# Kernel tuning notes

Hardware: AMD Instinct MI355X
Metric: run time of the kernel (lower is better)

Reference implementation:

```python
import jax, jax.numpy as jnp
import numpy as np

D_MODEL = 1024
N_HEADS = 16
D_K = D_MODEL // N_HEADS
RANK = 16
LORA_SCALING = 32.0 / RANK  # alpha / rank = 2.0
LN_EPS = 1e-5


def _lora_linear(x, w, b, A, B):
    # torch nn.Linear: x @ w.T + b ; LoRA: (x @ A @ B) * scaling
    return x @ w.T + b + (x @ A @ B) * LORA_SCALING


def setup_inputs() -> dict:
    key = jax.random.key(0)
    ks = jax.random.split(key, 20)
    d = {}
    d['x'] = jax.random.normal(ks[0], (4, 1024, D_MODEL), dtype=jnp.float32)
    i = 1
    for p in ('q', 'k', 'v', 'o'):
        d[f'{p}_w'] = jax.random.normal(ks[i], (D_MODEL, D_MODEL), dtype=jnp.float32) * (1.0 / np.sqrt(D_MODEL)); i += 1
        d[f'{p}_b'] = jax.random.normal(ks[i], (D_MODEL,), dtype=jnp.float32) * 0.01; i += 1
        d[f'{p}_A'] = jax.random.normal(ks[i], (D_MODEL, RANK), dtype=jnp.float32) * 0.01; i += 1
        d[f'{p}_B'] = jax.random.normal(ks[i], (RANK, D_MODEL), dtype=jnp.float32) * 0.01; i += 1
    d['ln_g'] = jnp.ones((D_MODEL,), dtype=jnp.float32)
    d['ln_b'] = jnp.zeros((D_MODEL,), dtype=jnp.float32)
    return d


def reference(x, q_w, q_b, q_A, q_B, k_w, k_b, k_A, k_B,
              v_w, v_b, v_A, v_B, o_w, o_b, o_A, o_B, ln_g, ln_b):
    B, S, _ = x.shape
    # QKV projections with LoRA, reshape to [B, H, S, d_k]
    def split_heads(t):
        return t.reshape(B, S, N_HEADS, D_K).transpose(0, 2, 1, 3)
    Q = split_heads(_lora_linear(x, q_w, q_b, q_A, q_B))
    K = split_heads(_lora_linear(x, k_w, k_b, k_A, k_B))
    V = split_heads(_lora_linear(x, v_w, v_b, v_A, v_B))

    scores = jnp.einsum('bhqd,bhkd->bhqk', Q, K) / jnp.sqrt(jnp.float32(D_K))
    attn = jax.nn.softmax(scores, axis=-1)  # dropout is identity in eval
    ctx = jnp.einsum('bhqk,bhkd->bhqd', attn, V)
    ctx = ctx.transpose(0, 2, 1, 3).reshape(B, S, D_MODEL)

    out = _lora_linear(ctx, o_w, o_b, o_A, o_B)
    # residual + LayerNorm
    h = out + x
    mu = jnp.mean(h, axis=-1, keepdims=True)
    var = jnp.mean(jnp.square(h - mu), axis=-1, keepdims=True)
    normed = (h - mu) * jax.lax.rsqrt(var + LN_EPS) * ln_g + ln_b
    return normed, attn.mean(axis=1)
```

## Files before the change

### kernel.cpp

```cpp
#include <hip/hip_runtime.h>

#define DMODEL 1024
#define NHEADS 16
#define DHEAD  64
#define RANK   16
#define BATCH  4
#define SEQ    1024
#define MTOT   (BATCH*SEQ)
#define QSCALE 0.18033688011112042f

typedef __bf16 bf16;
typedef __bf16 bf16x8 __attribute__((ext_vector_type(8)));
typedef __bf16 bf16x4 __attribute__((ext_vector_type(4)));
typedef float  f32x4  __attribute__((ext_vector_type(4)));

__device__ __forceinline__ int swz128(int row, int byte_in_row) {
  int slot = byte_in_row >> 4;
  return row * 128 + (((slot ^ (row & 7)) << 4) | (byte_in_row & 15));
}

__device__ __forceinline__ void gll16(const void* g, void* l) {
  __builtin_amdgcn_global_load_lds((const __attribute__((address_space(1))) unsigned int*)g,
                                   (__attribute__((address_space(3))) unsigned int*)l, 16, 0, 0);
}

#define TRRD(lo, hi, base, o0, o1)                                   \
  asm volatile("ds_read_b64_tr_b16 %0, %2 offset:" #o0 "\n\t"        \
               "ds_read_b64_tr_b16 %1, %2 offset:" #o1               \
               : "=v"(lo), "=v"(hi) : "v"(base));

__global__ void prep_weff_kernel(
    const float* __restrict__ W0, const float* __restrict__ A0, const float* __restrict__ B0,
    const float* __restrict__ W1, const float* __restrict__ A1, const float* __restrict__ B1,
    const float* __restrict__ W2, const float* __restrict__ A2, const float* __restrict__ B2,
    const float* __restrict__ W3, const float* __restrict__ A3, const float* __restrict__ B3,
    bf16* __restrict__ out) {
  const int l = blockIdx.y;
  const float* W = l == 0 ? W0 : l == 1 ? W1 : l == 2 ? W2 : W3;
  const float* A = l == 0 ? A0 : l == 1 ? A1 : l == 2 ? A2 : A3;
  const float* Bm = l == 0 ? B0 : l == 1 ? B1 : l == 2 ? B2 : B3;
  out += (size_t)l * DMODEL * DMODEL;
  const int n = blockIdx.x;
  __shared__ float bsc[RANK];
  if (threadIdx.x < RANK) bsc[threadIdx.x] = Bm[threadIdx.x * DMODEL + n] * 2.0f;
  __syncthreads();
  float br[RANK];
#pragma unroll
  for (int r = 0; r < RANK; ++r) br[r] = bsc[r];
  for (int k0 = 0; k0 < DMODEL; k0 += 256) {
    int k = k0 + threadIdx.x;
    float acc = W[n * DMODEL + k];
    const float4* arow = (const float4*)(A + k * RANK);
#pragma unroll
    for (int r4 = 0; r4 < 4; ++r4) {
      float4 a = arow[r4];
      acc += a.x*br[r4*4+0] + a.y*br[r4*4+1] + a.z*br[r4*4+2] + a.w*br[r4*4+3];
    }
    out[n * DMODEL + k] = (bf16)acc;
  }
}

__global__ void cast_x_kernel(const float* __restrict__ x, bf16* __restrict__ xb) {
  int i = (blockIdx.x * blockDim.x + threadIdx.x) * 4;
  float4 v = *(const float4*)(x + i);
  bf16x4 o = { (bf16)v.x, (bf16)v.y, (bf16)v.z, (bf16)v.w };
  *(bf16x4*)(xb + i) = o;
}

__device__ __forceinline__ void gemm_core64(
    const bf16* __restrict__ Ain, const bf16* __restrict__ Bin,
    char* sA, char* sB, int m0, int n0, f32x4 (&acc)[2][4]) {
  const int tid = threadIdx.x;
  const int w = tid >> 6, lane = tid & 63;
  const int wm = (w & 1) * 32, wn = (w >> 1) * 64;
  const bf16* pA[2]; char* lA[2];
  const bf16* pB[4]; char* lB[4];
#pragma unroll
  for (int i = 0; i < 2; ++i) {
    int chunk = i * 4 + w;
    int row = chunk * 8 + (lane >> 3);
    int ss = (lane & 7) ^ (row & 7);
    pA[i] = Ain + (size_t)(m0 + row) * DMODEL + ss * 8;
    lA[i] = sA + chunk * 1024;
  }
#pragma unroll
  for (int i = 0; i < 4; ++i) {
    int chunk = i * 4 + w;
    int row = chunk * 8 + (lane >> 3);
    int ss = (lane & 7) ^ (row & 7);
    pB[i] = Bin + (size_t)(n0 + row) * DMODEL + ss * 8;
    lB[i] = sB + chunk * 1024;
  }
  for (int kt = 0; kt < DMODEL / 64; ++kt) {
    const int kbase = kt * 64;
#pragma unroll
    for (int i = 0; i < 2; ++i) gll16(pA[i] + kbase, lA[i]);
#pragma unroll
    for (int i = 0; i < 4; ++i) gll16(pB[i] + kbase, lB[i]);
    __syncthreads();
#pragma unroll
    for (int ks = 0; ks < 2; ++ks) {
      bf16x8 af[2], bfg[4];
#pragma unroll
      for (int mi = 0; mi < 2; ++mi)
        af[mi] = *(const bf16x8*)(sA + swz128(wm + mi*16 + (lane & 15), ks*64 + (lane >> 4)*16));
#pragma unroll
      for (int ni = 0; ni < 4; ++ni)
        bfg[ni] = *(const bf16x8*)(sB + swz128(wn + ni*16 + (lane & 15), ks*64 + (lane >> 4)*16));
#pragma unroll
      for (int mi = 0; mi < 2; ++mi)
#pragma unroll
        for (int ni = 0; ni < 4; ++ni)
          acc[mi][ni] = __builtin_amdgcn_mfma_f32_16x16x32_bf16(af[mi], bfg[ni], acc[mi][ni], 0, 0, 0);
    }
    __syncthreads();
  }
}

__global__ __launch_bounds__(256) void gemm_qkv_kernel(
    const bf16* __restrict__ xb, const bf16* __restrict__ weff,
    const float* __restrict__ bq, const float* __restrict__ bk, const float* __restrict__ bv,
    bf16* __restrict__ Qb, bf16* __restrict__ Kb, bf16* __restrict__ Vb)
{
  __shared__ __align__(16) char sA[8192];
  __shared__ __align__(16) char sB[16384];
  const int tid = threadIdx.x, w = tid >> 6, lane = tid & 63;
  const int bid = blockIdx.x;
  const int nb = (bid & 7) * 192 + (bid >> 3);
  const int n0 = (nb % 24) * 128, m0 = (nb / 24) * 64;
  const int z = n0 >> 10;
  const float* bias = z == 0 ? bq : z == 1 ? bk : bv;
  bf16* outp = z == 0 ? Qb : (z == 1 ? Kb : Vb);
  const float scl = z == 0 ? QSCALE : 1.0f;
  const int wm = (w & 1) * 32, wn = (w >> 1) * 64;
  f32x4 acc[2][4] = {};
  gemm_core64(xb, weff, sA, sB, m0, n0, acc);
#pragma unroll
  for (int mi = 0; mi < 2; ++mi) {
#pragma unroll
    for (int ni = 0; ni < 4; ++ni) {
      int col = n0 + wn + ni * 16 + (lane & 15);
      float bcol = bias[col & 1023];
      int h = (col >> 6) & 15, d = col & 63;
#pragma unroll
      for (int r = 0; r < 4; ++r) {
        int row = m0 + wm + mi * 16 + (lane >> 4) * 4 + r;
        float v = (acc[mi][ni][r] + bcol) * scl;
        int b = row >> 10, s = row & 1023;
        outp[(size_t)((b * NHEADS + h) * SEQ + s) * DHEAD + d] = (bf16)v;
      }
    }
  }
}

__global__ __launch_bounds__(256) void gemm_o_kernel(
    const bf16* __restrict__ ctx, const bf16* __restrict__ weff,
    const float* __restrict__ bias, const float* __restrict__ resid,
    float* __restrict__ outf)
{
  __shared__ __align__(16) char sA[8192];
  __shared__ __align__(16) char sB[16384];
  const int tid = threadIdx.x, w = tid >> 6, lane = tid & 63;
  const int bid = blockIdx.x;
  const int nb = (bid & 7) * 64 + (bid >> 3);
  const int n0 = (nb & 7) * 128, m0 = (nb >> 3) * 64;
  const int wm = (w & 1) * 32, wn = (w >> 1) * 64;
  f32x4 acc[2][4] = {};
  gemm_core64(ctx, weff, sA, sB, m0, n0, acc);
#pragma unroll
  for (int mi = 0; mi < 2; ++mi) {
#pragma unroll
    for (int ni = 0; ni < 4; ++ni) {
      int col = n0 + wn + ni * 16 + (lane & 15);
      float bcol = bias[col];
#pragma unroll
      for (int r = 0; r < 4; ++r) {
        int row = m0 + wm + mi * 16 + (lane >> 4) * 4 + r;
        outf[(size_t)row * DMODEL + col] =
            acc[mi][ni][r] + bcol + resid[(size_t)row * DMODEL + col];
      }
    }
  }
}

__global__ __launch_bounds__(512) void flash_kernel(
    const bf16* __restrict__ Qb, const bf16* __restrict__ Kb, const bf16* __restrict__ Vb,
    bf16* __restrict__ ctx, float* __restrict__ lstat)
{
  __shared__ __align__(16) char sK[8192];
  __shared__ __align__(16) char sV[8192];
  __shared__ __align__(16) char sP[8 * 2048];
  const int tid = threadIdx.x, w = tid >> 6, lane = tid & 63;
  const int bid = blockIdx.x;
  const int nb = (bid & 7) * 64 + (bid >> 3);
  const int bh = nb >> 3;
  const int q0 = (nb & 7) * 128;
  const bf16* Qbase = Qb + (size_t)bh * SEQ * DHEAD;
  const bf16* Kbase = Kb + (size_t)bh * SEQ * DHEAD;
  const bf16* Vbase = Vb + (size_t)bh * SEQ * DHEAD;
  const int qw = q0 + w * 16;

  bf16x8 aq[2];
#pragma unroll
  for (int ks = 0; ks < 2; ++ks)
    aq[ks] = *(const bf16x8*)(Qbase + (size_t)(qw + (lane & 15)) * DHEAD + ks * 32 + (lane >> 4) * 8);

  const bf16* pK; const bf16* pV; char* lK; char* lV;
  {
    int ci = w;
    int rowK = ci * 8 + (lane >> 3);
    int ssK = (lane & 7) ^ (rowK & 7);
    pK = Kbase + (size_t)rowK * DHEAD + ssK * 8;
    lK = sK + ci * 1024;
    int kV = ci * 8 + ((lane >> 5) & 1) * 4 + ((lane >> 1) & 3);
    int dV = (((lane >> 3) & 3) << 4) + ((lane & 1) << 3);
    pV = Vbase + (size_t)kV * DHEAD + dV;
    lV = sV + ci * 1024;
  }

  char* sPw = sP + w * 2048;
  const unsigned pbase = (unsigned)(uintptr_t)sPw + ((lane >> 4) << 8) + ((lane & 15) << 3);
  const unsigned vbase0 = (unsigned)(uintptr_t)sV + ((lane >> 4) << 10) + ((lane & 15) << 3);
  char* pwr = sPw + ((lane >> 4) << 3) + (lane & 15) * 32;

  f32x4 cacc[4] = {};
  float lsum[4] = {0.f, 0.f, 0.f, 0.f};

  for (int kt = 0; kt < SEQ / 64; ++kt) {
    const size_t kofs = (size_t)(kt * 64) * DHEAD;
    gll16(pK + kofs, lK);
    gll16(pV + kofs, lV);
    __syncthreads();

    f32x4 sc[4] = {};
#pragma unroll
    for (int ks = 0; ks < 2; ++ks)
#pragma unroll
      for (int ni = 0; ni < 4; ++ni) {
        bf16x8 bk = *(const bf16x8*)(sK + swz128(ni*16 + (lane & 15), ks*64 + (lane >> 4)*16));
        sc[ni] = __builtin_amdgcn_mfma_f32_16x16x32_bf16(aq[ks], bk, sc[ni], 0, 0, 0);
      }

#pragma unroll
    for (int ni = 0; ni < 4; ++ni) {
      float p0 = __builtin_amdgcn_exp2f(sc[ni][0]);
      float p1 = __builtin_amdgcn_exp2f(sc[ni][1]);
      float p2 = __builtin_amdgcn_exp2f(sc[ni][2]);
      float p3 = __builtin_amdgcn_exp2f(sc[ni][3]);
      lsum[0] += p0; lsum[1] += p1; lsum[2] += p2; lsum[3] += p3;
      bf16x4 pb = { (bf16)p0, (bf16)p1, (bf16)p2, (bf16)p3 };
      *(bf16x4*)(pwr + ni * 512) = pb;
    }
    asm volatile("s_waitcnt lgkmcnt(0)" ::: "memory");

    unsigned long long t0, t1, v0[4], v1[4];
    TRRD(t0, t1, pbase, 0, 128)
    TRRD(v0[0], v1[0], vbase0, 0, 512)
    TRRD(v0[1], v1[1], vbase0, 128, 640)
    TRRD(v0[2], v1[2], vbase0, 256, 768)
    TRRD(v0[3], v1[3], vbase0, 384, 896)
    asm volatile("s_waitcnt lgkmcnt(0)" ::: "memory");
    __builtin_amdgcn_sched_barrier(0);
    {
      union { unsigned long long u[2]; bf16x8 v; } pu, vu;
      pu.u[0] = t0; pu.u[1] = t1;
#pragma unroll
      for (int ni = 0; ni < 4; ++ni) {
        vu.u[0] = v0[ni]; vu.u[1] = v1[ni];
        cacc[ni] = __builtin_amdgcn_mfma_f32_16x16x32_bf16(pu.v, vu.v, cacc[ni], 0, 0, 0);
      }
    }
    TRRD(t0, t1, pbase, 1024, 1152)
    TRRD(v0[0], v1[0], vbase0, 4096, 4608)
    TRRD(v0[1], v1[1], vbase0, 4224, 4736)
    TRRD(v0[2], v1[2], vbase0, 4352, 4864)
    TRRD(v0[3], v1[3], vbase0, 4480, 4992)
    asm volatile("s_waitcnt lgkmcnt(0)" ::: "memory");
    __builtin_amdgcn_sched_barrier(0);
    {
      union { unsigned long long u[2]; bf16x8 v; } pu, vu;
      pu.u[0] = t0; pu.u[1] = t1;
#pragma unroll
      for (int ni = 0; ni < 4; ++ni) {
        vu.u[0] = v0[ni]; vu.u[1] = v1[ni];
        cacc[ni] = __builtin_amdgcn_mfma_f32_16x16x32_bf16(pu.v, vu.v, cacc[ni], 0, 0, 0);
      }
    }
    __syncthreads();
  }

#pragma unroll
  for (int r = 0; r < 4; ++r) {
#pragma unroll
    for (int off = 1; off < 16; off <<= 1) lsum[r] += __shfl_xor(lsum[r], off);
  }

  const int b = bh >> 4, hh = bh & 15;
#pragma unroll
  for (int r = 0; r < 4; ++r) {
    float inv = __builtin_amdgcn_rcpf(lsum[r]);
    int qrow = qw + (lane >> 4) * 4 + r;
#pragma unroll
    for (int ni = 0; ni < 4; ++ni) {
      int d = ni * 16 + (lane & 15);
      ctx[(size_t)(b * SEQ + qrow) * DMODEL + hh * DHEAD + d] = (bf16)(cacc[ni][r] * inv);
    }
    if ((lane & 15) == 0) lstat[(size_t)bh * SEQ + qrow] = lsum[r];
  }
}

__global__ __launch_bounds__(256) void mean_kernel(
    const bf16* __restrict__ Qb, const bf16* __restrict__ Kb,
    const float* __restrict__ lstat, float* __restrict__ out2)
{
  __shared__ __align__(16) char sK[2 * 16384];
  const int tid = threadIdx.x, w = tid >> 6, lane = tid & 63;
  const int bid = blockIdx.x;
  const int nb2 = (bid & 7) * 64 + (bid >> 3);
  const int b = nb2 >> 7;
  const int q0 = ((nb2 >> 3) & 15) * 64, k0 = (nb2 & 7) * 128;
  const int qw = q0 + w * 16;
  size_t goff[4]; int lofs[4];
#pragma unroll
  for (int i = 0; i < 4; ++i) {
    int chunk = i * 4 + w;
    int row = chunk * 8 + (lane >> 3);
    int ss = (lane & 7) ^ (row & 7);
    goff[i] = (size_t)(k0 + row) * DHEAD + ss * 8;
    lofs[i] = chunk * 1024;
  }
  const bf16* Kb_b = Kb + (size_t)b * NHEADS * SEQ * DHEAD;
  const bf16* Qb_b = Qb + (size_t)b * NHEADS * SEQ * DHEAD;

  f32x4 macc[8] = {};
#pragma unroll
  for (int i = 0; i < 4; ++i) gll16(Kb_b + goff[i], sK + lofs[i]);
  asm volatile("s_waitcnt vmcnt(0)" ::: "memory");
  __syncthreads();

  for (int h = 0; h < NHEADS; ++h) {
    const int cur = (h & 1) << 14, nxt = cur ^ 16384;
    if (h + 1 < NHEADS) {
      const bf16* Kn = Kb_b + (size_t)(h + 1) * SEQ * DHEAD;
#pragma unroll
      for (int i = 0; i < 4; ++i) gll16(Kn + goff[i], sK + nxt + lofs[i]);
    }
    const bf16* Qbase = Qb_b + (size_t)h * SEQ * DHEAD;
    bf16x8 aq[2];
#pragma unroll
    for (int ks = 0; ks < 2; ++ks)
      aq[ks] = *(const bf16x8*)(Qbase + (size_t)(qw + (lane & 15)) * DHEAD
                                + ks * 32 + (lane >> 4) * 8);
    char* cK = sK + cur;
    f32x4 sc[8] = {};
#pragma unroll
    for (int ks = 0; ks < 2; ++ks)
#pragma unroll
      for (int ni = 0; ni < 8; ++ni) {
        bf16x8 bk = *(const bf16x8*)(cK + swz128(ni*16 + (lane & 15), ks*64 + (lane >> 4)*16));
        sc[ni] = __builtin_amdgcn_mfma_f32_16x16x32_bf16(aq[ks], bk, sc[ni], 0, 0, 0);
      }
    float lsc[4];
    const float* ls = lstat + ((size_t)(b * NHEADS + h)) * SEQ;
#pragma unroll
    for (int r = 0; r < 4; ++r)
      lsc[r] = 0.0625f * __builtin_amdgcn_rcpf(ls[qw + (lane >> 4)*4 + r]);
#pragma unroll
    for (int ni = 0; ni < 8; ++ni)
#pragma unroll
      for (int r = 0; r < 4; ++r)
        macc[ni][r] += __builtin_amdgcn_exp2f(sc[ni][r]) * lsc[r];
    asm volatile("s_waitcnt vmcnt(0)" ::: "memory");
    __syncthreads();
  }
#pragma unroll
  for (int r = 0; r < 4; ++r) {
    int qrow = qw + (lane >> 4) * 4 + r;
#pragma unroll
    for (int ni = 0; ni < 8; ++ni)
      out2[(size_t)(b * SEQ + qrow) * SEQ + k0 + ni * 16 + (lane & 15)] = macc[ni][r];
  }
}

__global__ __launch_bounds__(256) void ln_kernel(
    float* __restrict__ hb, const float* __restrict__ g,
    const float* __restrict__ bvec, float* __restrict__ out)
{
  const int row = blockIdx.x, t = threadIdx.x;
  float4 v = *(const float4*)(hb + (size_t)row * DMODEL + t * 4);
  float s = v.x + v.y + v.z + v.w;
  float s2 = v.x*v.x + v.y*v.y + v.z*v.z + v.w*v.w;
#pragma unroll
  for (int off = 32; off >= 1; off >>= 1) {
    s  += __shfl_down(s, off);
    s2 += __shfl_down(s2, off);
  }
  __shared__ float red[8];
  const int w = t >> 6;
  if ((t & 63) == 0) { red[w] = s; red[4 + w] = s2; }
  __syncthreads();
  if (t == 0) {
    red[0] = red[0] + red[1] + red[2] + red[3];
    red[4] = red[4] + red[5] + red[6] + red[7];
  }
  __syncthreads();
  float mu = red[0] * (1.0f / DMODEL);
  float var = red[4] * (1.0f / DMODEL) - mu * mu;
  float rs = rsqrtf(var + 1e-5f);
  float4 gv = *(const float4*)(g + t * 4);
  float4 bv = *(const float4*)(bvec + t * 4);
  float4 o;
  o.x = (v.x - mu) * rs * gv.x + bv.x;
  o.y = (v.y - mu) * rs * gv.y + bv.y;
  o.z = (v.z - mu) * rs * gv.z + bv.z;
  o.w = (v.w - mu) * rs * gv.w + bv.w;
  *(float4*)(out + (size_t)row * DMODEL + t * 4) = o;
}

extern "C" void kernel_launch(void* const* d_in, const int* in_sizes, int n_in,
                              void* d_out, int out_size, void* d_ws, size_t ws_size,
                              hipStream_t stream) {
  (void)in_sizes; (void)n_in; (void)out_size; (void)ws_size;
  const float* x = (const float*)d_in[0];
  const float* w_[4]  = {(const float*)d_in[1],  (const float*)d_in[5],
                         (const float*)d_in[9],  (const float*)d_in[13]};
  const float* b_[4]  = {(const float*)d_in[2],  (const float*)d_in[6],
                         (const float*)d_in[10], (const float*)d_in[14]};
  const float* A_[4]  = {(const float*)d_in[3],  (const float*)d_in[7],
                         (const float*)d_in[11], (const float*)d_in[15]};
  const float* Bm_[4] = {(const float*)d_in[4],  (const float*)d_in[8],
                         (const float*)d_in[12], (const float*)d_in[16]};
  const float* lng = (const float*)d_in[17];
  const float* lnb = (const float*)d_in[18];

  char* ws = (char*)d_ws;
  bf16* xb    = (bf16*)(ws);
  bf16* weff  = (bf16*)(ws + (8u  << 20));
  bf16* Qb    = (bf16*)(ws + (16u << 20));
  bf16* Kb    = (bf16*)(ws + (24u << 20));
  bf16* Vb    = (bf16*)(ws + (32u << 20));
  float* lstat = (float*)(ws + (40u << 20));
  bf16* ctx = xb;
  float* hbuf = (float*)d_out;
  float* out2 = (float*)d_out + (size_t)MTOT * DMODEL;

  prep_weff_kernel<<<dim3(DMODEL, 4), dim3(256), 0, stream>>>(
      w_[0], A_[0], Bm_[0], w_[1], A_[1], Bm_[1],
      w_[2], A_[2], Bm_[2], w_[3], A_[3], Bm_[3], weff);
  cast_x_kernel<<<dim3(MTOT * DMODEL / 1024), dim3(256), 0, stream>>>(x, xb);

  gemm_qkv_kernel<<<dim3(1536), 256, 0, stream>>>(
      xb, weff, b_[0], b_[1], b_[2], Qb, Kb, Vb);

  flash_kernel<<<dim3(512), 512, 0, stream>>>(Qb, Kb, Vb, ctx, lstat);
  mean_kernel<<<dim3(512), 256, 0, stream>>>(Qb, Kb, lstat, out2);
  gemm_o_kernel<<<dim3(512), 256, 0, stream>>>(
      ctx, weff + 3u * DMODEL * DMODEL, b_[3], x, hbuf);
  ln_kernel<<<dim3(MTOT), 256, 0, stream>>>(hbuf, lng, lnb, hbuf);
}
```

Before: 144.5 us.

## Double-buffer K/V tiles in flash kernel and enlarge QKV GEMM tile

The flash attention kernel now keeps two LDS buffers for K and V. It prefetches the next 64-key tile with global_load_lds while the current tile is consumed, which hides global load latency and removes one barrier per iteration. The QKV projection GEMM moves from a 64x128 tile with 256 threads to a 128x128 tile with 512 threads (8 waves). That raises operand reuse per block and halves the grid. The cost is doubled LDS use in flash (32 KB extra) and fewer, larger GEMM blocks, which may lower occupancy.

Result: no change. 142.9 us (-1.1%).

```diff
diff --git a/kernel.cpp b/kernel.cpp
--- a/kernel.cpp
+++ b/kernel.cpp
@@ -67,6 +67,79 @@
   *(bf16x4*)(xb + i) = o;
 }
 
+__global__ __launch_bounds__(512) void gemm_qkv_kernel(
+    const bf16* __restrict__ xb, const bf16* __restrict__ weff,
+    const float* __restrict__ bq, const float* __restrict__ bk, const float* __restrict__ bv,
+    bf16* __restrict__ Qb, bf16* __restrict__ Kb, bf16* __restrict__ Vb)
+{
+  __shared__ __align__(16) char sA[16384];
+  __shared__ __align__(16) char sB[16384];
+  const int tid = threadIdx.x, w = tid >> 6, lane = tid & 63;
+  const int bid = blockIdx.x;
+  const int nb = (bid & 7) * 96 + (bid >> 3);
+  const int n0 = (nb % 24) * 128, m0 = (nb / 24) * 128;
+  const int z = n0 >> 10;
+  const float* bias = z == 0 ? bq : z == 1 ? bk : bv;
+  bf16* outp = z == 0 ? Qb : (z == 1 ? Kb : Vb);
+  const float scl = z == 0 ? QSCALE : 1.0f;
+  const int wm = (w & 3) * 32, wn = (w >> 2) * 64;
+  f32x4 acc[2][4] = {};
+
+  const bf16* pA[2]; const bf16* pB[2]; char* lA[2]; char* lB[2];
+#pragma unroll
+  for (int i = 0; i < 2; ++i) {
+    int ci = i * 8 + w;
+    int row = ci * 8 + (lane >> 3);
+    int ss = (lane & 7) ^ (row & 7);
+    pA[i] = xb + (size_t)(m0 + row) * DMODEL + ss * 8;
+    pB[i] = weff + (size_t)(n0 + row) * DMODEL + ss * 8;
+    lA[i] = sA + ci * 1024;
+    lB[i] = sB + ci * 1024;
+  }
+  for (int kt = 0; kt < DMODEL / 64; ++kt) {
+    const int kbase = kt * 64;
+#pragma unroll
+    for (int i = 0; i < 2; ++i) {
+      gll16(pA[i] + kbase, lA[i]);
+      gll16(pB[i] + kbase, lB[i]);
+    }
+    __syncthreads();
+#pragma unroll
+    for (int ks = 0; ks < 2; ++ks) {
+      bf16x8 af[2], bfg[4];
+#pragma unroll
+      for (int mi = 0; mi < 2; ++mi)
+        af[mi] = *(const bf16x8*)(sA + swz128(wm + mi*16 + (lane & 15), ks*64 + (lane >> 4)*16));
+#pragma unroll
+      for (int ni = 0; ni < 4; ++ni)
+        bfg[ni] = *(const bf16x8*)(sB + swz128(wn + ni*16 + (lane & 15), ks*64 + (lane >> 4)*16));
+#pragma unroll
+      for (int mi = 0; mi < 2; ++mi)
+#pragma unroll
+        for (int ni = 0; ni < 4; ++ni)
+          acc[mi][ni] = __builtin_amdgcn_mfma_f32_16x16x32_bf16(af[mi], bfg[ni], acc[mi][ni], 0, 0, 0);
+    }
+    __syncthreads();
+  }
+
+#pragma unroll
+  for (int mi = 0; mi < 2; ++mi) {
+#pragma unroll
+    for (int ni = 0; ni < 4; ++ni) {
+      int col = n0 + wn + ni * 16 + (lane & 15);
+      float bcol = bias[col & 1023];
+      int h = (col >> 6) & 15, d = col & 63;
+#pragma unroll
+      for (int r = 0; r < 4; ++r) {
+        int row = m0 + wm + mi * 16 + (lane >> 4) * 4 + r;
+        float v = (acc[mi][ni][r] + bcol) * scl;
+        int b = row >> 10, s = row & 1023;
+        outp[(size_t)((b * NHEADS + h) * SEQ + s) * DHEAD + d] = (bf16)v;
+      }
+    }
+  }
+}
+
 __device__ __forceinline__ void gemm_core64(
     const bf16* __restrict__ Ain, const bf16* __restrict__ Bin,
     char* sA, char* sB, int m0, int n0, f32x4 (&acc)[2][4]) {
@@ -114,42 +187,6 @@
           acc[mi][ni] = __builtin_amdgcn_mfma_f32_16x16x32_bf16(af[mi], bfg[ni], acc[mi][ni], 0, 0, 0);
     }
     __syncthreads();
-  }
-}
-
-__global__ __launch_bounds__(256) void gemm_qkv_kernel(
-    const bf16* __restrict__ xb, const bf16* __restrict__ weff,
-    const float* __restrict__ bq, const float* __restrict__ bk, const float* __restrict__ bv,
-    bf16* __restrict__ Qb, bf16* __restrict__ Kb, bf16* __restrict__ Vb)
-{
-  __shared__ __align__(16) char sA[8192];
-  __shared__ __align__(16) char sB[16384];
-  const int tid = threadIdx.x, w = tid >> 6, lane = tid & 63;
-  const int bid = blockIdx.x;
-  const int nb = (bid & 7) * 192 + (bid >> 3);
-  const int n0 = (nb % 24) * 128, m0 = (nb / 24) * 64;
-  const int z = n0 >> 10;
-  const float* bias = z == 0 ? bq : z == 1 ? bk : bv;
-  bf16* outp = z == 0 ? Qb : (z == 1 ? Kb : Vb);
-  const float scl = z == 0 ? QSCALE : 1.0f;
-  const int wm = (w & 1) * 32, wn = (w >> 1) * 64;
-  f32x4 acc[2][4] = {};
-  gemm_core64(xb, weff, sA, sB, m0, n0, acc);
-#pragma unroll
-  for (int mi = 0; mi < 2; ++mi) {
-#pragma unroll
-    for (int ni = 0; ni < 4; ++ni) {
-      int col = n0 + wn + ni * 16 + (lane & 15);
-      float bcol = bias[col & 1023];
-      int h = (col >> 6) & 15, d = col & 63;
-#pragma unroll
-      for (int r = 0; r < 4; ++r) {
-        int row = m0 + wm + mi * 16 + (lane >> 4) * 4 + r;
-        float v = (acc[mi][ni][r] + bcol) * scl;
-        int b = row >> 10, s = row & 1023;
-        outp[(size_t)((b * NHEADS + h) * SEQ + s) * DHEAD + d] = (bf16)v;
-      }
-    }
   }
 }
 
@@ -187,8 +224,8 @@
     const bf16* __restrict__ Qb, const bf16* __restrict__ Kb, const bf16* __restrict__ Vb,
     bf16* __restrict__ ctx, float* __restrict__ lstat)
 {
-  __shared__ __align__(16) char sK[8192];
-  __shared__ __align__(16) char sV[8192];
+  __shared__ __align__(16) char sK[2 * 8192];
+  __shared__ __align__(16) char sV[2 * 8192];
   __shared__ __align__(16) char sP[8 * 2048];
   const int tid = threadIdx.x, w = tid >> 6, lane = tid & 63;
   const int bid = blockIdx.x;
@@ -205,17 +242,17 @@
   for (int ks = 0; ks < 2; ++ks)
     aq[ks] = *(const bf16x8*)(Qbase + (size_t)(qw + (lane & 15)) * DHEAD + ks * 32 + (lane >> 4) * 8);
 
-  const bf16* pK; const bf16* pV; char* lK; char* lV;
+  const bf16* pK; const bf16* pV; int lKo; int lVo;
   {
     int ci = w;
     int rowK = ci * 8 + (lane >> 3);
     int ssK = (lane & 7) ^ (rowK & 7);
     pK = Kbase + (size_t)rowK * DHEAD + ssK * 8;
-    lK = sK + ci * 1024;
+    lKo = ci * 1024;
     int kV = ci * 8 + ((lane >> 5) & 1) * 4 + ((lane >> 1) & 3);
     int dV = (((lane >> 3) & 3) << 4) + ((lane & 1) << 3);
     pV = Vbase + (size_t)kV * DHEAD + dV;
-    lV = sV + ci * 1024;
+    lVo = ci * 1024;
   }
 
   char* sPw = sP + w * 2048;
@@ -226,18 +263,24 @@
   f32x4 cacc[4] = {};
   float lsum[4] = {0.f, 0.f, 0.f, 0.f};
 
+  gll16(pK, sK + lKo);
+  gll16(pV, sV + lVo);
+  __syncthreads();
+
   for (int kt = 0; kt < SEQ / 64; ++kt) {
-    const size_t kofs = (size_t)(kt * 64) * DHEAD;
-    gll16(pK + kofs, lK);
-    gll16(pV + kofs, lV);
-    __syncthreads();
+    const int cur = (kt & 1) << 13, nxt = cur ^ 8192;
+    if (kt + 1 < SEQ / 64) {
+      const size_t kofs = (size_t)((kt + 1) * 64) * DHEAD;
+      gll16(pK + kofs, sK + nxt + lKo);
+      gll16(pV + kofs, sV + nxt + lVo);
+    }
 
     f32x4 sc[4] = {};
 #pragma unroll
     for (int ks = 0; ks < 2; ++ks)
 #pragma unroll
       for (int ni = 0; ni < 4; ++ni) {
-        bf16x8 bk = *(const bf16x8*)(sK + swz128(ni*16 + (lane & 15), ks*64 + (lane >> 4)*16));
+        bf16x8 bk = *(const bf16x8*)(sK + cur + swz128(ni*16 + (lane & 15), ks*64 + (lane >> 4)*16));
         sc[ni] = __builtin_amdgcn_mfma_f32_16x16x32_bf16(aq[ks], bk, sc[ni], 0, 0, 0);
       }
 
@@ -254,11 +297,12 @@
     asm volatile("s_waitcnt lgkmcnt(0)" ::: "memory");
 
     unsigned long long t0, t1, v0[4], v1[4];
+    const unsigned vb = vbase0 + cur;
     TRRD(t0, t1, pbase, 0, 128)
-    TRRD(v0[0], v1[0], vbase0, 0, 512)
-    TRRD(v0[1], v1[1], vbase0, 128, 640)
-    TRRD(v0[2], v1[2], vbase0, 256, 768)
-    TRRD(v0[3], v1[3], vbase0, 384, 896)
+    TRRD(v0[0], v1[0], vb, 0, 512)
+    TRRD(v0[1], v1[1], vb, 128, 640)
+    TRRD(v0[2], v1[2], vb, 256, 768)
+    TRRD(v0[3], v1[3], vb, 384, 896)
     asm volatile("s_waitcnt lgkmcnt(0)" ::: "memory");
     __builtin_amdgcn_sched_barrier(0);
     {
@@ -271,10 +315,10 @@
       }
     }
     TRRD(t0, t1, pbase, 1024, 1152)
-    TRRD(v0[0], v1[0], vbase0, 4096, 4608)
-    TRRD(v0[1], v1[1], vbase0, 4224, 4736)
-    TRRD(v0[2], v1[2], vbase0, 4352, 4864)
-    TRRD(v0[3], v1[3], vbase0, 4480, 4992)
+    TRRD(v0[0], v1[0], vb, 4096, 4608)
+    TRRD(v0[1], v1[1], vb, 4224, 4736)
+    TRRD(v0[2], v1[2], vb, 4352, 4864)
+    TRRD(v0[3], v1[3], vb, 4480, 4992)
     asm volatile("s_waitcnt lgkmcnt(0)" ::: "memory");
     __builtin_amdgcn_sched_barrier(0);
     {
@@ -449,7 +493,7 @@
       w_[2], A_[2], Bm_[2], w_[3], A_[3], Bm_[3], weff);
   cast_x_kernel<<<dim3(MTOT * DMODEL / 1024), dim3(256), 0, stream>>>(x, xb);
 
-  gemm_qkv_kernel<<<dim3(1536), 256, 0, stream>>>(
+  gemm_qkv_kernel<<<dim3(768), 512, 0, stream>>>(
       xb, weff, b_[0], b_[1], b_[2], Qb, Kb, Vb);
 
   flash_kernel<<<dim3(512), 512, 0, stream>>>(Qb, Kb, Vb, ctx, lstat);
```
